# Kernel optimization log

Hardware: AMD Instinct MI355X
Metric: run time of the kernel (lower is better)

Reference implementation:

```python
import jax, jax.numpy as jnp
import numpy as np

B, T, D, E = 8, 4096, 128, 16
TOP_K = 2


def setup_inputs() -> dict:
    key = jax.random.key(0)
    k1, k2, k3 = jax.random.split(key, 3)
    x = jax.random.normal(k1, (B, T, D), dtype=jnp.float32)
    Wg = jax.random.normal(k2, (D, E), dtype=jnp.float32) * 0.08   # gate Dense kernel
    bg = jnp.zeros((E,), dtype=jnp.float32)                         # gate Dense bias
    Ew = jax.random.normal(k3, (E, D, D), dtype=jnp.float32) * (1.0 / np.sqrt(D))  # expert weights
    return {"x": x, "Wg": Wg, "bg": bg, "Ew": Ew}


def reference(x, Wg, bg, Ew):
    # gate: Dense(n_experts, softmax) on x (context defaults to x)
    gate_scores = jax.nn.softmax(x @ Wg + bg, axis=-1)              # (B,T,E)
    top_vals, top_idx = jax.lax.top_k(gate_scores, TOP_K)           # (B,T,2)
    top_w = top_vals / (jnp.sum(top_vals, axis=-1, keepdims=True) + 1e-6)
    # all-expert transform (faithful to original dense einsum)
    expert_outputs = jnp.einsum('btd,edo->bteo', x, Ew)             # (B,T,E,D)
    # combine top-k one-hot masks with normalized weights -> per-expert weight
    onehot = jax.nn.one_hot(top_idx, E, dtype=x.dtype)              # (B,T,2,E)
    mask = jnp.sum(onehot * top_w[..., None], axis=2)               # (B,T,E)
    m = mask[..., None]                                             # (B,T,E,1)
    weighted_avg = jnp.sum(expert_outputs * m, axis=2)              # (B,T,D)
    diff_sq = jnp.square(expert_outputs - weighted_avg[:, :, None, :])
    weighted_var = jnp.sum(diff_sq * m, axis=2)                     # (B,T,D)
    consensus = jnp.exp(-jnp.mean(weighted_var, axis=-1))           # (B,T)
    return (weighted_avg, consensus)
```

## Files before the change

### kernel.cpp

```cpp
#include <hip/hip_runtime.h>
#include <hip/hip_bf16.h>

#define NTOK 32768
#define DD 128
#define NE 16
#define CSTRIDE 32

#define OFF_COUNTS 0
#define OFF_TOKW   (4*1024)
#define OFF_LISTS  (512*1024)
#define OFF_XB     (3*1024*1024)
#define OFF_EWT    (11*1024*1024)
#define OFF_YBUF   (12*1024*1024)

typedef __attribute__((ext_vector_type(8))) short bf16x8;
typedef __attribute__((ext_vector_type(4))) float f32x4;

static __device__ inline ushort f2bf(float f) {
    uint u = __builtin_bit_cast(uint, f);
    u = u + 0x7FFFu + ((u >> 16) & 1u);
    return (ushort)(u >> 16);
}
static __device__ inline float b2f(ushort h) {
    uint u = ((uint)h) << 16;
    return __builtin_bit_cast(float, u);
}

__global__ __launch_bounds__(256) void ewt_kernel(
    const float* __restrict__ Ew, ushort* __restrict__ ewT)
{
    __shared__ float tile[32][33];
    const int b = blockIdx.x;
    const int e = b >> 4, ki = ((b >> 2) & 3) * 32, oi = (b & 3) * 32;
    const int tid = threadIdx.x;
    const int r = tid >> 3, c4 = (tid & 7) * 4;
    const float4 v = *(const float4*)(Ew + (size_t)e * DD * DD + (ki + r) * DD + oi + c4);
    tile[r][c4 + 0] = v.x; tile[r][c4 + 1] = v.y;
    tile[r][c4 + 2] = v.z; tile[r][c4 + 3] = v.w;
    __syncthreads();
    const int o = tid >> 3, k4 = (tid & 7) * 4;
    ushort4 s;
    s.x = f2bf(tile[k4 + 0][o]);
    s.y = f2bf(tile[k4 + 1][o]);
    s.z = f2bf(tile[k4 + 2][o]);
    s.w = f2bf(tile[k4 + 3][o]);
    *(ushort4*)(ewT + (size_t)e * DD * DD + (oi + o) * DD + ki + k4) = s;
}

__global__ __launch_bounds__(256) void gate_kernel(
    const float* __restrict__ x, const float* __restrict__ Wg,
    const float* __restrict__ bg,
    int* __restrict__ counts, int* __restrict__ lists, float* __restrict__ tokw,
    ushort* __restrict__ xb)
{
    __shared__ float sWg[DD * NE];
    __shared__ float sBg[NE];
    __shared__ int   sCnt[NE];
    __shared__ int   sBase[NE];
    const int tid = threadIdx.x;
    for (int i = tid; i < DD * NE; i += 256) sWg[i] = Wg[i];
    if (tid < NE) { sBg[tid] = bg[tid]; sCnt[tid] = 0; }
    __syncthreads();

    const int t = blockIdx.x * 64 + (tid >> 2);
    const int g = tid & 3;
    const float* xt = x + (size_t)t * DD;
    ushort*      xo = xb + (size_t)t * DD;

    float logits[NE];
    #pragma unroll
    for (int e = 0; e < NE; ++e) logits[e] = 0.0f;

    #pragma unroll
    for (int i = 0; i < 8; ++i) {
        const int d0 = g * 4 + i * 16;
        float4 v = ((const float4*)xt)[g + i * 4];
        const float* w0 = &sWg[(d0 + 0) * NE];
        const float* w1 = &sWg[(d0 + 1) * NE];
        const float* w2 = &sWg[(d0 + 2) * NE];
        const float* w3 = &sWg[(d0 + 3) * NE];
        #pragma unroll
        for (int e = 0; e < NE; ++e) {
            float a = logits[e];
            a = fmaf(v.x, w0[e], a);
            a = fmaf(v.y, w1[e], a);
            a = fmaf(v.z, w2[e], a);
            a = fmaf(v.w, w3[e], a);
            logits[e] = a;
        }
        ushort4 s; s.x = f2bf(v.x); s.y = f2bf(v.y); s.z = f2bf(v.z); s.w = f2bf(v.w);
        *(ushort4*)(xo + d0) = s;
    }

    #pragma unroll
    for (int e = 0; e < NE; ++e) {
        float a = logits[e];
        a += __shfl_xor(a, 1);
        a += __shfl_xor(a, 2);
        logits[e] = a + sBg[e];
    }

    float m = logits[0];
    #pragma unroll
    for (int e = 1; e < NE; ++e) m = fmaxf(m, logits[e]);
    float Z = 0.0f;
    #pragma unroll
    for (int e = 0; e < NE; ++e) Z += expf(logits[e] - m);

    int i1 = 0; float l1 = logits[0];
    #pragma unroll
    for (int e = 1; e < NE; ++e) if (logits[e] > l1) { l1 = logits[e]; i1 = e; }
    int i2 = -1; float l2 = -3.4e38f;
    #pragma unroll
    for (int e = 0; e < NE; ++e) if (e != i1 && logits[e] > l2) { l2 = logits[e]; i2 = e; }

    int s1 = 0, s2 = 0;
    if (g == 0) {
        float p1 = expf(l1 - m) / Z;
        float p2 = expf(l2 - m) / Z;
        float s  = p1 + p2 + 1e-6f;
        tokw[t * 2 + 0] = p1 / s;
        tokw[t * 2 + 1] = p2 / s;
        s1 = atomicAdd(&sCnt[i1], 1);
        s2 = atomicAdd(&sCnt[i2], 1);
    }
    __syncthreads();
    if (tid < NE) sBase[tid] = atomicAdd(&counts[tid * CSTRIDE], sCnt[tid]);
    __syncthreads();
    if (g == 0) {
        lists[i1 * NTOK + sBase[i1] + s1] = t * 2 + 0;
        lists[i2 * NTOK + sBase[i2] + s2] = t * 2 + 1;
    }
}

__global__ __launch_bounds__(256) void expert_kernel(
    const ushort* __restrict__ xb, const ushort* __restrict__ ewT,
    const int* __restrict__ counts, const int* __restrict__ lists,
    ushort* __restrict__ ybuf)
{
    const int e = blockIdx.y;
    const int count = counts[e * CSTRIDE];
    const int start = blockIdx.x * 64;
    if (start >= count) return;

    const int tid  = threadIdx.x;
    const int lane = tid & 63, wv = tid >> 6;
    const int row  = lane & 15;
    const int kg   = lane >> 4;

    const int idx = start + wv * 16 + row;
    const int en  = (idx < count) ? lists[e * NTOK + idx] : -1;
    const ushort* xrow = xb + (size_t)((en < 0 ? 0 : en) >> 1) * DD;

    bf16x8 xf[4];
    #pragma unroll
    for (int k = 0; k < 4; ++k)
        xf[k] = *(const bf16x8*)(xrow + k * 32 + kg * 8);

    const ushort* ewe = ewT + (size_t)e * DD * DD;
    f32x4 acc[8];
    #pragma unroll
    for (int n = 0; n < 8; ++n) acc[n] = (f32x4)(0.0f);

    #pragma unroll
    for (int n = 0; n < 8; ++n) {
        const ushort* er = ewe + (size_t)(n * 16 + row) * DD + kg * 8;
        #pragma unroll
        for (int k = 0; k < 4; ++k) {
            bf16x8 ef = *(const bf16x8*)(er + k * 32);
            acc[n] = __builtin_amdgcn_mfma_f32_16x16x32_bf16(ef, xf[k], acc[n], 0, 0, 0);
        }
    }

    if (en >= 0) {
        ushort* yr = ybuf + (size_t)en * DD + kg * 4;
        #pragma unroll
        for (int n = 0; n < 8; ++n) {
            ushort4 s;
            s.x = f2bf(acc[n][0]); s.y = f2bf(acc[n][1]);
            s.z = f2bf(acc[n][2]); s.w = f2bf(acc[n][3]);
            *(ushort4*)(yr + n * 16) = s;
        }
    }
}

__global__ __launch_bounds__(256) void combine_kernel(
    const ushort* __restrict__ ybuf, const float* __restrict__ tokw,
    float* __restrict__ avg_out, float* __restrict__ cons_out)
{
    const int tid = threadIdx.x;
    const int lane = tid & 63, wv = tid >> 6;
    const int half = lane >> 5, hl = lane & 31;
    const int t0 = blockIdx.x * 16 + wv * 4;

    #pragma unroll
    for (int j = 0; j < 4; ++j) {
        const int t = t0 + j;
        const float w1 = tokw[t * 2 + 0];
        const float w2 = tokw[t * 2 + 1];
        const float wo = half ? w2 : w1;
        const float wx = half ? w1 : w2;

        ushort4 raw = *(const ushort4*)(ybuf + (size_t)(t * 2 + half) * DD + hl * 4);
        float o0 = b2f(raw.x), o1 = b2f(raw.y), o2 = b2f(raw.z), o3 = b2f(raw.w);
        float x0 = __shfl_xor(o0, 32);
        float x1 = __shfl_xor(o1, 32);
        float x2 = __shfl_xor(o2, 32);
        float x3 = __shfl_xor(o3, 32);

        float a0 = wo * o0 + wx * x0;
        float a1 = wo * o1 + wx * x1;
        float a2 = wo * o2 + wx * x2;
        float a3 = wo * o3 + wx * x3;
        if (half == 0) {
            float4 av; av.x = a0; av.y = a1; av.z = a2; av.w = a3;
            ((float4*)(avg_out + (size_t)t * DD))[hl] = av;
        }
        float d0 = o0 - a0, d1 = o1 - a1, d2 = o2 - a2, d3 = o3 - a3;
        float e0 = x0 - a0, e1 = x1 - a1, e2 = x2 - a2, e3 = x3 - a3;
        float v = wo * (d0*d0 + d1*d1 + d2*d2 + d3*d3)
                + wx * (e0*e0 + e1*e1 + e2*e2 + e3*e3);
        v += __shfl_xor(v, 1);
        v += __shfl_xor(v, 2);
        v += __shfl_xor(v, 4);
        v += __shfl_xor(v, 8);
        v += __shfl_xor(v, 16);
        if (lane == 0) cons_out[t] = expf(-v * (1.0f / 128.0f));
    }
}

extern "C" void kernel_launch(void* const* d_in, const int* in_sizes, int n_in,
                              void* d_out, int out_size, void* d_ws, size_t ws_size,
                              hipStream_t stream)
{
    const float* x  = (const float*)d_in[0];
    const float* Wg = (const float*)d_in[1];
    const float* bg = (const float*)d_in[2];
    const float* Ew = (const float*)d_in[3];
    float* out = (float*)d_out;

    char* ws = (char*)d_ws;
    int*    counts = (int*)(ws + OFF_COUNTS);
    float*  tokw   = (float*)(ws + OFF_TOKW);
    int*    lists  = (int*)(ws + OFF_LISTS);
    ushort* xbuf   = (ushort*)(ws + OFF_XB);
    ushort* ewT    = (ushort*)(ws + OFF_EWT);
    ushort* ybuf   = (ushort*)(ws + OFF_YBUF);

    hipMemsetAsync(counts, 0, NE * CSTRIDE * sizeof(int), stream);

    ewt_kernel<<<256, 256, 0, stream>>>(Ew, ewT);
    gate_kernel<<<NTOK / 64, 256, 0, stream>>>(x, Wg, bg, counts, lists, tokw, xbuf);
    expert_kernel<<<dim3(NTOK / 64, NE), 256, 0, stream>>>(xbuf, ewT, counts, lists, ybuf);
    combine_kernel<<<NTOK / 16, 256, 0, stream>>>(ybuf, tokw, out, out + (size_t)NTOK * DD);
}
```

Baseline: 125.0 us.

## Bucket tokens by expert pair and fuse expert GEMM with combine

The gate now bins each token by its ordered (top1, top2) expert pair, giving 256 buckets instead of 16 per-expert lists. A single fused kernel runs both experts' GEMMs per bucket tile and computes the weighted average and consensus in registers. This removes the bf16 intermediate y buffer, its write and read, and the separate combine launch. In exchange it uses 4 persistent-ish blocks per pair with uneven bucket sizes, quadruple accumulator sets (higher register pressure), and a larger lists buffer.

```diff
diff --git a/kernel.cpp b/kernel.cpp
--- a/kernel.cpp
+++ b/kernel.cpp
@@ -4,14 +4,14 @@
 #define NTOK 32768
 #define DD 128
 #define NE 16
+#define NPAIR 256
 #define CSTRIDE 32
 
 #define OFF_COUNTS 0
-#define OFF_TOKW   (4*1024)
-#define OFF_LISTS  (512*1024)
-#define OFF_XB     (3*1024*1024)
-#define OFF_EWT    (11*1024*1024)
-#define OFF_YBUF   (12*1024*1024)
+#define OFF_TOKW   (64*1024)
+#define OFF_XB     (1*1024*1024)
+#define OFF_EWT    (9*1024*1024)
+#define OFF_LISTS  (16*1024*1024)
 
 typedef __attribute__((ext_vector_type(8))) short bf16x8;
 typedef __attribute__((ext_vector_type(4))) float f32x4;
@@ -20,10 +20,6 @@
     uint u = __builtin_bit_cast(uint, f);
     u = u + 0x7FFFu + ((u >> 16) & 1u);
     return (ushort)(u >> 16);
-}
-static __device__ inline float b2f(ushort h) {
-    uint u = ((uint)h) << 16;
-    return __builtin_bit_cast(float, u);
 }
 
 __global__ __launch_bounds__(256) void ewt_kernel(
@@ -55,11 +51,12 @@
 {
     __shared__ float sWg[DD * NE];
     __shared__ float sBg[NE];
-    __shared__ int   sCnt[NE];
-    __shared__ int   sBase[NE];
+    __shared__ int   sCnt[NPAIR];
+    __shared__ int   sBase[NPAIR];
     const int tid = threadIdx.x;
     for (int i = tid; i < DD * NE; i += 256) sWg[i] = Wg[i];
-    if (tid < NE) { sBg[tid] = bg[tid]; sCnt[tid] = 0; }
+    if (tid < NE) sBg[tid] = bg[tid];
+    sCnt[tid] = 0;
     __syncthreads();
 
     const int t = blockIdx.x * 64 + (tid >> 2);
@@ -114,118 +111,108 @@
     #pragma unroll
     for (int e = 0; e < NE; ++e) if (e != i1 && logits[e] > l2) { l2 = logits[e]; i2 = e; }
 
-    int s1 = 0, s2 = 0;
+    int slot = 0, pair = 0;
     if (g == 0) {
         float p1 = expf(l1 - m) / Z;
         float p2 = expf(l2 - m) / Z;
         float s  = p1 + p2 + 1e-6f;
         tokw[t * 2 + 0] = p1 / s;
         tokw[t * 2 + 1] = p2 / s;
-        s1 = atomicAdd(&sCnt[i1], 1);
-        s2 = atomicAdd(&sCnt[i2], 1);
-    }
-    __syncthreads();
-    if (tid < NE) sBase[tid] = atomicAdd(&counts[tid * CSTRIDE], sCnt[tid]);
-    __syncthreads();
-    if (g == 0) {
-        lists[i1 * NTOK + sBase[i1] + s1] = t * 2 + 0;
-        lists[i2 * NTOK + sBase[i2] + s2] = t * 2 + 1;
-    }
-}
-
-__global__ __launch_bounds__(256) void expert_kernel(
+        pair = i1 * NE + i2;
+        slot = atomicAdd(&sCnt[pair], 1);
+    }
+    __syncthreads();
+    if (sCnt[tid] > 0) sBase[tid] = atomicAdd(&counts[tid * CSTRIDE], sCnt[tid]);
+    __syncthreads();
+    if (g == 0)
+        lists[pair * NTOK + sBase[pair] + slot] = t;
+}
+
+__global__ __launch_bounds__(256) void moe_kernel(
     const ushort* __restrict__ xb, const ushort* __restrict__ ewT,
     const int* __restrict__ counts, const int* __restrict__ lists,
-    ushort* __restrict__ ybuf)
-{
-    const int e = blockIdx.y;
-    const int count = counts[e * CSTRIDE];
-    const int start = blockIdx.x * 64;
-    if (start >= count) return;
+    const float* __restrict__ tokw,
+    float* __restrict__ avg_out, float* __restrict__ cons_out)
+{
+    const int pair = blockIdx.y;
+    const int ea = pair >> 4, eb = pair & 15;
+    const int count = counts[pair * CSTRIDE];
 
     const int tid  = threadIdx.x;
     const int lane = tid & 63, wv = tid >> 6;
     const int row  = lane & 15;
     const int kg   = lane >> 4;
 
-    const int idx = start + wv * 16 + row;
-    const int en  = (idx < count) ? lists[e * NTOK + idx] : -1;
-    const ushort* xrow = xb + (size_t)((en < 0 ? 0 : en) >> 1) * DD;
-
-    bf16x8 xf[4];
-    #pragma unroll
-    for (int k = 0; k < 4; ++k)
-        xf[k] = *(const bf16x8*)(xrow + k * 32 + kg * 8);
-
-    const ushort* ewe = ewT + (size_t)e * DD * DD;
-    f32x4 acc[8];
-    #pragma unroll
-    for (int n = 0; n < 8; ++n) acc[n] = (f32x4)(0.0f);
-
-    #pragma unroll
-    for (int n = 0; n < 8; ++n) {
-        const ushort* er = ewe + (size_t)(n * 16 + row) * DD + kg * 8;
+    const ushort* ewa = ewT + (size_t)ea * DD * DD;
+    const ushort* ewb = ewT + (size_t)eb * DD * DD;
+
+    for (int tile = blockIdx.x; tile * 128 < count; tile += 4) {
+        const int base = tile * 128 + wv * 32;
+        const int idx0 = base + row, idx1 = base + 16 + row;
+        const int t0 = (idx0 < count) ? lists[pair * NTOK + idx0] : -1;
+        const int t1 = (idx1 < count) ? lists[pair * NTOK + idx1] : -1;
+
+        const ushort* xr0 = xb + (size_t)(t0 < 0 ? 0 : t0) * DD;
+        const ushort* xr1 = xb + (size_t)(t1 < 0 ? 0 : t1) * DD;
+        bf16x8 xf0[4], xf1[4];
         #pragma unroll
         for (int k = 0; k < 4; ++k) {
-            bf16x8 ef = *(const bf16x8*)(er + k * 32);
-            acc[n] = __builtin_amdgcn_mfma_f32_16x16x32_bf16(ef, xf[k], acc[n], 0, 0, 0);
-        }
-    }
-
-    if (en >= 0) {
-        ushort* yr = ybuf + (size_t)en * DD + kg * 4;
+            xf0[k] = *(const bf16x8*)(xr0 + k * 32 + kg * 8);
+            xf1[k] = *(const bf16x8*)(xr1 + k * 32 + kg * 8);
+        }
+        const int tw0 = (t0 < 0 ? 0 : t0), tw1 = (t1 < 0 ? 0 : t1);
+        const float w1a = tokw[tw0 * 2 + 0], w2a = tokw[tw0 * 2 + 1];
+        const float w1b = tokw[tw1 * 2 + 0], w2b = tokw[tw1 * 2 + 1];
+
+        f32x4 aA0[8], aA1[8], aB0[8], aB1[8];
         #pragma unroll
         for (int n = 0; n < 8; ++n) {
-            ushort4 s;
-            s.x = f2bf(acc[n][0]); s.y = f2bf(acc[n][1]);
-            s.z = f2bf(acc[n][2]); s.w = f2bf(acc[n][3]);
-            *(ushort4*)(yr + n * 16) = s;
-        }
-    }
-}
-
-__global__ __launch_bounds__(256) void combine_kernel(
-    const ushort* __restrict__ ybuf, const float* __restrict__ tokw,
-    float* __restrict__ avg_out, float* __restrict__ cons_out)
-{
-    const int tid = threadIdx.x;
-    const int lane = tid & 63, wv = tid >> 6;
-    const int half = lane >> 5, hl = lane & 31;
-    const int t0 = blockIdx.x * 16 + wv * 4;
-
-    #pragma unroll
-    for (int j = 0; j < 4; ++j) {
-        const int t = t0 + j;
-        const float w1 = tokw[t * 2 + 0];
-        const float w2 = tokw[t * 2 + 1];
-        const float wo = half ? w2 : w1;
-        const float wx = half ? w1 : w2;
-
-        ushort4 raw = *(const ushort4*)(ybuf + (size_t)(t * 2 + half) * DD + hl * 4);
-        float o0 = b2f(raw.x), o1 = b2f(raw.y), o2 = b2f(raw.z), o3 = b2f(raw.w);
-        float x0 = __shfl_xor(o0, 32);
-        float x1 = __shfl_xor(o1, 32);
-        float x2 = __shfl_xor(o2, 32);
-        float x3 = __shfl_xor(o3, 32);
-
-        float a0 = wo * o0 + wx * x0;
-        float a1 = wo * o1 + wx * x1;
-        float a2 = wo * o2 + wx * x2;
-        float a3 = wo * o3 + wx * x3;
-        if (half == 0) {
-            float4 av; av.x = a0; av.y = a1; av.z = a2; av.w = a3;
-            ((float4*)(avg_out + (size_t)t * DD))[hl] = av;
-        }
-        float d0 = o0 - a0, d1 = o1 - a1, d2 = o2 - a2, d3 = o3 - a3;
-        float e0 = x0 - a0, e1 = x1 - a1, e2 = x2 - a2, e3 = x3 - a3;
-        float v = wo * (d0*d0 + d1*d1 + d2*d2 + d3*d3)
-                + wx * (e0*e0 + e1*e1 + e2*e2 + e3*e3);
-        v += __shfl_xor(v, 1);
-        v += __shfl_xor(v, 2);
-        v += __shfl_xor(v, 4);
-        v += __shfl_xor(v, 8);
-        v += __shfl_xor(v, 16);
-        if (lane == 0) cons_out[t] = expf(-v * (1.0f / 128.0f));
+            aA0[n] = (f32x4)(0.0f); aA1[n] = (f32x4)(0.0f);
+            aB0[n] = (f32x4)(0.0f); aB1[n] = (f32x4)(0.0f);
+        }
+
+        #pragma unroll
+        for (int n = 0; n < 8; ++n) {
+            const ushort* ra = ewa + (size_t)(n * 16 + row) * DD + kg * 8;
+            const ushort* rb = ewb + (size_t)(n * 16 + row) * DD + kg * 8;
+            #pragma unroll
+            for (int k = 0; k < 4; ++k) {
+                bf16x8 efa = *(const bf16x8*)(ra + k * 32);
+                bf16x8 efb = *(const bf16x8*)(rb + k * 32);
+                aA0[n] = __builtin_amdgcn_mfma_f32_16x16x32_bf16(efa, xf0[k], aA0[n], 0, 0, 0);
+                aA1[n] = __builtin_amdgcn_mfma_f32_16x16x32_bf16(efa, xf1[k], aA1[n], 0, 0, 0);
+                aB0[n] = __builtin_amdgcn_mfma_f32_16x16x32_bf16(efb, xf0[k], aB0[n], 0, 0, 0);
+                aB1[n] = __builtin_amdgcn_mfma_f32_16x16x32_bf16(efb, xf1[k], aB1[n], 0, 0, 0);
+            }
+        }
+
+        float v0 = 0.0f, v1 = 0.0f;
+        #pragma unroll
+        for (int n = 0; n < 8; ++n) {
+            float4 av0, av1;
+            float* p0 = (float*)&av0; float* p1 = (float*)&av1;
+            #pragma unroll
+            for (int r = 0; r < 4; ++r) {
+                float yA = aA0[n][r], yB = aB0[n][r];
+                float a = w1a * yA + w2a * yB;
+                p0[r] = a;
+                float dA = yA - a, dB = yB - a;
+                v0 = fmaf(w1a, dA * dA, fmaf(w2a, dB * dB, v0));
+                float zA = aA1[n][r], zB = aB1[n][r];
+                float b = w1b * zA + w2b * zB;
+                p1[r] = b;
+                float eA = zA - b, eB = zB - b;
+                v1 = fmaf(w1b, eA * eA, fmaf(w2b, eB * eB, v1));
+            }
+            if (t0 >= 0) *(float4*)(avg_out + (size_t)t0 * DD + n * 16 + kg * 4) = av0;
+            if (t1 >= 0) *(float4*)(avg_out + (size_t)t1 * DD + n * 16 + kg * 4) = av1;
+        }
+        v0 += __shfl_xor(v0, 16); v0 += __shfl_xor(v0, 32);
+        v1 += __shfl_xor(v1, 16); v1 += __shfl_xor(v1, 32);
+        if (kg == 0) {
+            if (t0 >= 0) cons_out[t0] = expf(-v0 * (1.0f / 128.0f));
+            if (t1 >= 0) cons_out[t1] = expf(-v1 * (1.0f / 128.0f));
+        }
     }
 }
 
@@ -242,15 +229,14 @@
     char* ws = (char*)d_ws;
     int*    counts = (int*)(ws + OFF_COUNTS);
     float*  tokw   = (float*)(ws + OFF_TOKW);
-    int*    lists  = (int*)(ws + OFF_LISTS);
     ushort* xbuf   = (ushort*)(ws + OFF_XB);
     ushort* ewT    = (ushort*)(ws + OFF_EWT);
-    ushort* ybuf   = (ushort*)(ws + OFF_YBUF);
-
-    hipMemsetAsync(counts, 0, NE * CSTRIDE * sizeof(int), stream);
+    int*    lists  = (int*)(ws + OFF_LISTS);
+
+    hipMemsetAsync(counts, 0, NPAIR * CSTRIDE * sizeof(int), stream);
 
     ewt_kernel<<<256, 256, 0, stream>>>(Ew, ewT);
     gate_kernel<<<NTOK / 64, 256, 0, stream>>>(x, Wg, bg, counts, lists, tokw, xbuf);
-    expert_kernel<<<dim3(NTOK / 64, NE), 256, 0, stream>>>(xbuf, ewT, counts, lists, ybuf);
-    combine_kernel<<<NTOK / 16, 256, 0, stream>>>(ybuf, tokw, out, out + (size_t)NTOK * DD);
-}
+    moe_kernel<<<dim3(4, NPAIR), 256, 0, stream>>>(xbuf, ewT, counts, lists, tokw,
+                                                   out, out + (size_t)NTOK * DD);
+}
```

Result: slower. 167.1 us (+33.6%).
